# Kernel optimization log

Hardware: AMD Instinct MI355X
Metric: run time of the kernel (lower is better)

Reference implementation:

```python
import jax, jax.numpy as jnp
import numpy as np

BS, LX, LY, D, H, DK = 2, 2048, 2048, 1024, 16, 64


def setup_inputs() -> dict:
    key = jax.random.key(0)
    ks = jax.random.split(key, 12)
    s = 1.0 / np.sqrt(D)
    return {
        "x": jax.random.normal(ks[0], (BS, LX, D), jnp.float32),
        "y": jax.random.normal(ks[1], (BS, LY, D), jnp.float32),
        "mask": jnp.zeros((BS, 1, LX, LY), jnp.float32),
        "Wq": jax.random.normal(ks[2], (D, H * DK), jnp.float32) * s,
        "bq": jnp.zeros((H * DK,), jnp.float32),
        "Wk": jax.random.normal(ks[3], (D, H * DK), jnp.float32) * s,
        "bk": jnp.zeros((H * DK,), jnp.float32),
        "Wv": jax.random.normal(ks[4], (D, H * DK), jnp.float32) * s,
        "bv": jnp.zeros((H * DK,), jnp.float32),
        "Wo": jax.random.normal(ks[5], (H * DK, D), jnp.float32) * s,
        "bo": jnp.zeros((D,), jnp.float32),
    }


def reference(x, y, mask, Wq, bq, Wk, bk, Wv, bv, Wo, bo):
    bs, lx, _ = x.shape
    ly = y.shape[1]
    norm = DK ** 0.5
    # projections -> (bs, len, H, DK)
    q = (x @ Wq + bq).reshape(bs, lx, H, DK)
    k = (y @ Wk + bk).reshape(bs, ly, H, DK)
    v = (y @ Wv + bv).reshape(bs, ly, H, DK)
    # scores: (bs, H, lx, ly)
    scores = jnp.einsum('bxhd,byhd->bhxy', q, k) / norm + mask
    attn = jax.nn.softmax(scores, axis=-1)
    # output: (bs, lx, H, DK) -> (bs, lx, H*DK)
    out = jnp.einsum('bhxy,byhd->bxhd', attn, v).reshape(bs, lx, H * DK)
    return out @ Wo + bo
```

## Files before the change

kernel.cpp:

```cpp
#include <hip/hip_runtime.h>
#include <hip/hip_bf16.h>


typedef __bf16 bf16;
typedef __bf16 bf16x4 __attribute__((ext_vector_type(4)));
typedef __bf16 bf16x8 __attribute__((ext_vector_type(8)));
typedef float floatx4 __attribute__((ext_vector_type(4)));

#define MFMA16(a, b, c) __builtin_amdgcn_mfma_f32_16x16x32_bf16(a, b, c, 0, 0, 0)

constexpr int BS = 2, LX = 2048, LY = 2048, D = 1024, H = 16, DK = 64;
constexpr int HD = H * DK;
constexpr float LOG2E = 1.4426950408889634f;

__device__ __forceinline__ void cp16(const bf16* g, bf16* l) {
  __builtin_amdgcn_global_load_lds(
      (const __attribute__((address_space(1))) unsigned int*)g,
      (__attribute__((address_space(3))) unsigned int*)l, 16, 0, 0);
}

__global__ __launch_bounds__(256) void wprep(const float* __restrict__ W0, bf16* __restrict__ T0,
                                             const float* __restrict__ W1, bf16* __restrict__ T1,
                                             const float* __restrict__ W2, bf16* __restrict__ T2,
                                             const float* __restrict__ W3, bf16* __restrict__ T3) {
  __shared__ bf16 tile[64][72];
  const float* W;
  bf16* T;
  switch (blockIdx.z) {
    case 0: W = W0; T = T0; break;
    case 1: W = W1; T = T1; break;
    case 2: W = W2; T = T2; break;
    default: W = W3; T = T3; break;
  }
  const int kt = blockIdx.x, nt = blockIdx.y;
  const int t = threadIdx.x;
  const int r = t >> 2, c4 = (t & 3) * 16;
  const float* src = W + (size_t)(kt * 64 + r) * 1024 + nt * 64 + c4;
#pragma unroll
  for (int i = 0; i < 16; i++) tile[r][c4 + i] = (bf16)src[i];
  __syncthreads();
  bf16 vals[16];
#pragma unroll
  for (int i = 0; i < 16; i++) vals[i] = tile[c4 + i][r];
  bf16* dst = T + (size_t)(nt * 64 + r) * 1024 + kt * 64 + c4;
#pragma unroll
  for (int i = 0; i < 16; i++) dst[i] = vals[i];
}

__global__ __launch_bounds__(256) void convbf(const float* __restrict__ x, bf16* __restrict__ xb,
                                              const float* __restrict__ y, bf16* __restrict__ yb) {
  const float* src = blockIdx.y ? y : x;
  bf16* dst = blockIdx.y ? yb : xb;
  const size_t i = ((size_t)blockIdx.x * 256 + threadIdx.x) * 8;
  float4 a = *(const float4*)(src + i);
  float4 c = *(const float4*)(src + i + 4);
  bf16 tmp[8] = {(bf16)a.x, (bf16)a.y, (bf16)a.z, (bf16)a.w,
                 (bf16)c.x, (bf16)c.y, (bf16)c.z, (bf16)c.w};
  *(bf16x8*)(dst + i) = *(const bf16x8*)tmp;
}

__global__ __launch_bounds__(256) void maskscan(const float* __restrict__ mask, int* __restrict__ flags) {
  const int region = blockIdx.x >> 5, sub = blockIdx.x & 31;
  const float4* p = (const float4*)mask + (size_t)region * 65536 + sub * 2048;
  bool nz = false;
#pragma unroll
  for (int it = 0; it < 8; it++) {
    float4 v = p[it * 256 + threadIdx.x];
    nz |= (v.x != 0.f) | (v.y != 0.f) | (v.z != 0.f) | (v.w != 0.f);
  }
  if (nz) atomicOr(&flags[region], 1);
}

__global__ __launch_bounds__(256) void qkv_gemm(const bf16* __restrict__ xb, const bf16* __restrict__ yb,
                                                const bf16* __restrict__ Wtq, const bf16* __restrict__ Wtk,
                                                const bf16* __restrict__ Wtv,
                                                const float* __restrict__ bq, const float* __restrict__ bk,
                                                const float* __restrict__ bv,
                                                bf16* __restrict__ Qb, bf16* __restrict__ Kb,
                                                bf16* __restrict__ Vt) {
  constexpr int K = 1024, N = 1024;
  __shared__ __align__(16) bf16 smem[128 * 136];
  bf16* As = smem;
  bf16* Bs = smem + 128 * 64;
  bf16* Ct = smem;

  const int z = blockIdx.z;
  const bf16* A = (z == 0) ? xb : yb;
  const bf16* Bt = (z == 0) ? Wtq : (z == 1) ? Wtk : Wtv;
  const float* bias = (z == 0) ? bq : (z == 1) ? bk : bv;

  const int t = threadIdx.x;
  const int w = t >> 6, lane = t & 63, quad = lane >> 4, l15 = lane & 15;
  const int wr = (w & 1) * 64, wc = (w >> 1) * 64;
  const int mbase = blockIdx.y * 128, nbase = blockIdx.x * 128;
  const int srow = lane >> 3, schunk = (lane & 7) ^ srow;

  floatx4 acc[4][4] = {};

  for (int k0 = 0; k0 < K; k0 += 64) {
    __syncthreads();
#pragma unroll
    for (int j = 0; j < 4; j++) {
      const int r0 = w * 32 + j * 8;
      cp16(A + (size_t)(mbase + r0 + srow) * K + k0 + schunk * 8, As + r0 * 64);
      cp16(Bt + (size_t)(nbase + r0 + srow) * K + k0 + schunk * 8, Bs + r0 * 64);
    }
    __syncthreads();
    bf16x8 af[4][2], bfr[4][2];
#pragma unroll
    for (int i = 0; i < 4; i++) {
      const int ra = wr + i * 16 + l15;
      const int sa = quad ^ (ra & 7);
      af[i][0] = *(const bf16x8*)&As[ra * 64 + sa * 8];
      af[i][1] = *(const bf16x8*)&As[ra * 64 + (sa ^ 4) * 8];
      const int rb = wc + i * 16 + l15;
      const int sb = quad ^ (rb & 7);
      bfr[i][0] = *(const bf16x8*)&Bs[rb * 64 + sb * 8];
      bfr[i][1] = *(const bf16x8*)&Bs[rb * 64 + (sb ^ 4) * 8];
    }
#pragma unroll
    for (int i = 0; i < 4; i++)
#pragma unroll
      for (int jn = 0; jn < 4; jn++) {
        acc[i][jn] = MFMA16(af[i][0], bfr[jn][0], acc[i][jn]);
        acc[i][jn] = MFMA16(af[i][1], bfr[jn][1], acc[i][jn]);
      }
  }

  if (z <= 1) {
    bf16* outp = (z == 0) ? Qb : Kb;
    const float sc = (z == 0) ? 0.125f * LOG2E : 1.0f;
#pragma unroll
    for (int jn = 0; jn < 4; jn++) {
      const int n = nbase + wc + jn * 16 + l15;
      const float bv2 = bias[n];
#pragma unroll
      for (int i = 0; i < 4; i++)
#pragma unroll
        for (int r = 0; r < 4; r++) {
          const int m = mbase + wr + i * 16 + quad * 4 + r;
          outp[(size_t)m * N + n] = (bf16)((acc[i][jn][r] + bv2) * sc);
        }
    }
  } else {
    __syncthreads();
#pragma unroll
    for (int jn = 0; jn < 4; jn++) {
      const int nl = wc + jn * 16 + l15;
      const float bv2 = bias[nbase + nl];
#pragma unroll
      for (int i = 0; i < 4; i++)
#pragma unroll
        for (int r = 0; r < 4; r++) {
          const int ml = wr + i * 16 + quad * 4 + r;
          Ct[nl * 136 + ml] = (bf16)(acc[i][jn][r] + bv2);
        }
    }
    __syncthreads();
    const int n = t >> 1, mh = (t & 1) * 64;
    const int gn = nbase + n;
    const int hh = gn >> 6, dk = gn & 63;
    const int bb = mbase >> 11, y0 = (mbase & 2047) + mh;
    bf16* dst = Vt + ((size_t)(bb * H + hh) * DK + dk) * LY + y0;
    const bf16* srcr = &Ct[n * 136 + mh];
#pragma unroll
    for (int u = 0; u < 8; u++) *(bf16x8*)(dst + u * 8) = *(const bf16x8*)(srcr + u * 8);
  }
}

__global__ __launch_bounds__(256) void out_gemm(const bf16* __restrict__ A, const bf16* __restrict__ Bt,
                                                const float* __restrict__ bias, float* __restrict__ outp) {
  constexpr int K = 1024, N = 1024;
  __shared__ __align__(16) bf16 As[128 * 64];
  __shared__ __align__(16) bf16 Bs[128 * 64];
  const int t = threadIdx.x;
  const int w = t >> 6, lane = t & 63, quad = lane >> 4, l15 = lane & 15;
  const int wr = (w & 1) * 64, wc = (w >> 1) * 64;
  const int mbase = blockIdx.y * 128, nbase = blockIdx.x * 128;
  const int srow = lane >> 3, schunk = (lane & 7) ^ srow;

  floatx4 acc[4][4] = {};
  for (int k0 = 0; k0 < K; k0 += 64) {
    __syncthreads();
#pragma unroll
    for (int j = 0; j < 4; j++) {
      const int r0 = w * 32 + j * 8;
      cp16(A + (size_t)(mbase + r0 + srow) * K + k0 + schunk * 8, As + r0 * 64);
      cp16(Bt + (size_t)(nbase + r0 + srow) * K + k0 + schunk * 8, Bs + r0 * 64);
    }
    __syncthreads();
    bf16x8 af[4][2], bfr[4][2];
#pragma unroll
    for (int i = 0; i < 4; i++) {
      const int ra = wr + i * 16 + l15;
      const int sa = quad ^ (ra & 7);
      af[i][0] = *(const bf16x8*)&As[ra * 64 + sa * 8];
      af[i][1] = *(const bf16x8*)&As[ra * 64 + (sa ^ 4) * 8];
      const int rb = wc + i * 16 + l15;
      const int sb = quad ^ (rb & 7);
      bfr[i][0] = *(const bf16x8*)&Bs[rb * 64 + sb * 8];
      bfr[i][1] = *(const bf16x8*)&Bs[rb * 64 + (sb ^ 4) * 8];
    }
#pragma unroll
    for (int i = 0; i < 4; i++)
#pragma unroll
      for (int jn = 0; jn < 4; jn++) {
        acc[i][jn] = MFMA16(af[i][0], bfr[jn][0], acc[i][jn]);
        acc[i][jn] = MFMA16(af[i][1], bfr[jn][1], acc[i][jn]);
      }
  }
#pragma unroll
  for (int jn = 0; jn < 4; jn++) {
    const int n = nbase + wc + jn * 16 + l15;
    const float bv2 = bias[n];
#pragma unroll
    for (int i = 0; i < 4; i++)
#pragma unroll
      for (int r = 0; r < 4; r++) {
        const int m = mbase + wr + i * 16 + quad * 4 + r;
        outp[(size_t)m * N + n] = acc[i][jn][r] + bv2;
      }
  }
}

__global__ __launch_bounds__(256, 2) void attn4(const bf16* __restrict__ Q, const bf16* __restrict__ Kb,
                                                const bf16* __restrict__ Vt, const float* __restrict__ mask,
                                                const int* __restrict__ flags, bf16* __restrict__ Hout) {
  __shared__ __align__(16) bf16 Ks[2][64 * 64];
  __shared__ __align__(16) bf16 Vs[2][64 * 64];
  __shared__ __align__(16) bf16 Plds[4][32 * 72];
  const int t = threadIdx.x;
  const int w = t >> 6, lane = t & 63, quad = lane >> 4, l15 = lane & 15;
  const int xt = blockIdx.x, h = blockIdx.y, b = blockIdx.z;
  const int qbase = xt * 128 + w * 32;
  const int srow = lane >> 3, schunk = (lane & 7) ^ srow;

  bf16x8 qf[2][2];
#pragma unroll
  for (int rt = 0; rt < 2; rt++) {
    const bf16* qrow = Q + (size_t)(b * LX + qbase + rt * 16 + l15) * HD + h * DK;
    qf[rt][0] = *(const bf16x8*)(qrow + quad * 8);
    qf[rt][1] = *(const bf16x8*)(qrow + 32 + quad * 8);
  }
  const int mflag = flags[b * 16 + xt];

  bf16 onearr[8];
#pragma unroll
  for (int i = 0; i < 8; i++) onearr[i] = (bf16)((l15 == 0) ? 1.0f : 0.0f);
  const bf16x8 onesf = *(const bf16x8*)onearr;

  floatx4 o[2][4] = {};
  floatx4 ol[2] = {};

  const bf16* Kbase = Kb + (size_t)b * LY * HD + h * DK;
  const bf16* Vbase = Vt + (size_t)(b * H + h) * DK * LY;

#define STAGE(yt, bufi)                                                               \
  {                                                                                   \
    _Pragma("unroll") for (int j = 0; j < 2; j++) {                                   \
      const int r0 = w * 16 + j * 8;                                                  \
      cp16(Kbase + (size_t)((yt) + r0 + srow) * HD + schunk * 8, &Ks[bufi][r0 * 64]); \
      cp16(Vbase + (size_t)(r0 + srow) * LY + (yt) + schunk * 8, &Vs[bufi][r0 * 64]); \
    }                                                                                 \
  }

  STAGE(0, 0);

  int buf = 0;
  for (int yt = 0; yt < LY; yt += 64) {
    __syncthreads();
    if (yt + 64 < LY) STAGE(yt + 64, buf ^ 1);

    bf16x8 kf[4][2];
#pragma unroll
    for (int nt = 0; nt < 4; nt++) {
      const int ry = nt * 16 + l15;
      const int sk = quad ^ (ry & 7);
      kf[nt][0] = *(const bf16x8*)&Ks[buf][ry * 64 + sk * 8];
      kf[nt][1] = *(const bf16x8*)&Ks[buf][ry * 64 + (sk ^ 4) * 8];
    }
    floatx4 s[2][4] = {};
#pragma unroll
    for (int nt = 0; nt < 4; nt++)
#pragma unroll
      for (int rt = 0; rt < 2; rt++) {
        s[rt][nt] = MFMA16(kf[nt][0], qf[rt][0], s[rt][nt]);
        s[rt][nt] = MFMA16(kf[nt][1], qf[rt][1], s[rt][nt]);
      }
    if (mflag) {
#pragma unroll
      for (int rt = 0; rt < 2; rt++)
#pragma unroll
        for (int nt = 0; nt < 4; nt++) {
          const float* mp =
              mask + (size_t)(b * LX + qbase + rt * 16 + l15) * LY + yt + nt * 16 + quad * 4;
          float4 mv = *(const float4*)mp;
          s[rt][nt][0] = fminf(s[rt][nt][0] + LOG2E * mv.x, 30.f);
          s[rt][nt][1] = fminf(s[rt][nt][1] + LOG2E * mv.y, 30.f);
          s[rt][nt][2] = fminf(s[rt][nt][2] + LOG2E * mv.z, 30.f);
          s[rt][nt][3] = fminf(s[rt][nt][3] + LOG2E * mv.w, 30.f);
        }
    }

#pragma unroll
    for (int rt = 0; rt < 2; rt++)
#pragma unroll
      for (int nt = 0; nt < 4; nt++) {
        bf16x4 pk;
#pragma unroll
        for (int r = 0; r < 4; r++) pk[r] = (bf16)exp2f(s[rt][nt][r]);
        *(bf16x4*)&Plds[w][(rt * 16 + l15) * 72 + nt * 16 + quad * 4] = pk;
      }

    bf16x8 pf[2][2];
#pragma unroll
    for (int rt = 0; rt < 2; rt++) {
      const bf16* prow = &Plds[w][(rt * 16 + l15) * 72];
      pf[rt][0] = *(const bf16x8*)(prow + quad * 8);
      pf[rt][1] = *(const bf16x8*)(prow + 32 + quad * 8);
    }
#pragma unroll
    for (int u = 0; u < 4; u++) {
      const int rd = u * 16 + l15;
      const int sv = quad ^ (rd & 7);
      bf16x8 v0 = *(const bf16x8*)&Vs[buf][rd * 64 + sv * 8];
      bf16x8 v1 = *(const bf16x8*)&Vs[buf][rd * 64 + (sv ^ 4) * 8];
#pragma unroll
      for (int rt = 0; rt < 2; rt++) {
        o[rt][u] = MFMA16(pf[rt][0], v0, o[rt][u]);
        o[rt][u] = MFMA16(pf[rt][1], v1, o[rt][u]);
      }
    }
#pragma unroll
    for (int rt = 0; rt < 2; rt++) {
      ol[rt] = MFMA16(pf[rt][0], onesf, ol[rt]);
      ol[rt] = MFMA16(pf[rt][1], onesf, ol[rt]);
    }
    buf ^= 1;
  }

#pragma unroll
  for (int rt = 0; rt < 2; rt++)
#pragma unroll
    for (int r = 0; r < 4; r++) {
      const float lsum = __shfl(ol[rt][r], lane & 48, 64);
      const float rl = 1.0f / lsum;
      const int m = b * LX + qbase + rt * 16 + quad * 4 + r;
#pragma unroll
      for (int u = 0; u < 4; u++)
        Hout[(size_t)m * HD + h * DK + u * 16 + l15] = (bf16)(o[rt][u][r] * rl);
    }
#undef STAGE
}

extern "C" void kernel_launch(void* const* d_in, const int* in_sizes, int n_in,
                              void* d_out, int out_size, void* d_ws, size_t ws_size,
                              hipStream_t stream) {
  const float* x = (const float*)d_in[0];
  const float* y = (const float*)d_in[1];
  const float* mask = (const float*)d_in[2];
  const float* Wq = (const float*)d_in[3];
  const float* bq = (const float*)d_in[4];
  const float* Wk = (const float*)d_in[5];
  const float* bk = (const float*)d_in[6];
  const float* Wv = (const float*)d_in[7];
  const float* bv = (const float*)d_in[8];
  const float* Wo = (const float*)d_in[9];
  const float* bo = (const float*)d_in[10];

  char* ws = (char*)d_ws;
  size_t off = 0;
  bf16* Qb = (bf16*)(ws + off); off += (size_t)BS * LX * HD * 2;
  bf16* Kb = (bf16*)(ws + off); off += (size_t)BS * LY * HD * 2;
  bf16* Vt = (bf16*)(ws + off); off += (size_t)BS * LY * HD * 2;
  bf16* Hb = (bf16*)(ws + off); off += (size_t)BS * LX * HD * 2;
  bf16* xbf = (bf16*)(ws + off); off += (size_t)BS * LX * D * 2;
  bf16* ybf = (bf16*)(ws + off); off += (size_t)BS * LY * D * 2;
  bf16* Wtq = (bf16*)(ws + off); off += (size_t)D * HD * 2;
  bf16* Wtk = (bf16*)(ws + off); off += (size_t)D * HD * 2;
  bf16* Wtv = (bf16*)(ws + off); off += (size_t)D * HD * 2;
  bf16* Wto = (bf16*)(ws + off); off += (size_t)HD * D * 2;
  int* flags = (int*)(ws + off); off += 32 * sizeof(int);

  dim3 blk(256);
  wprep<<<dim3(16, 16, 4), blk, 0, stream>>>(Wq, Wtq, Wk, Wtk, Wv, Wtv, Wo, Wto);
  convbf<<<dim3(2048, 2), blk, 0, stream>>>(x, xbf, y, ybf);
  hipMemsetAsync(flags, 0, 32 * sizeof(int), stream);
  maskscan<<<dim3(1024), blk, 0, stream>>>(mask, flags);
  qkv_gemm<<<dim3(8, 32, 3), blk, 0, stream>>>(xbf, ybf, Wtq, Wtk, Wtv, bq, bk, bv, Qb, Kb, Vt);
  attn4<<<dim3(16, 16, 2), blk, 0, stream>>>(Qb, Kb, Vt, mask, flags, Hb);
  out_gemm<<<dim3(8, 32), blk, 0, stream>>>(Hb, Wto, bo, (float*)d_out);
}
```

Before: 264.0 us.

## Fuse prep kernels, retile out GEMM, unroll attention loop by two buffers

Merges the weight transpose, activation bf16 conversion and mask scan into one prep kernel to cut launch overhead. Shrinks the output GEMM N-tile from 128 to 64, doubling the grid for better CU occupancy. Unrolls the attention loop into two static-buffer tile calls so buffer indices become compile-time, and hoists swizzle and mask base address computations. The smaller out_gemm tile lowers data reuse per block.

```diff
diff --git a/kernel.cpp b/kernel.cpp
--- a/kernel.cpp
+++ b/kernel.cpp
@@ -19,56 +19,59 @@
       (__attribute__((address_space(3))) unsigned int*)l, 16, 0, 0);
 }
 
-__global__ __launch_bounds__(256) void wprep(const float* __restrict__ W0, bf16* __restrict__ T0,
-                                             const float* __restrict__ W1, bf16* __restrict__ T1,
-                                             const float* __restrict__ W2, bf16* __restrict__ T2,
-                                             const float* __restrict__ W3, bf16* __restrict__ T3) {
-  __shared__ bf16 tile[64][72];
-  const float* W;
-  bf16* T;
-  switch (blockIdx.z) {
-    case 0: W = W0; T = T0; break;
-    case 1: W = W1; T = T1; break;
-    case 2: W = W2; T = T2; break;
-    default: W = W3; T = T3; break;
-  }
-  const int kt = blockIdx.x, nt = blockIdx.y;
+__global__ __launch_bounds__(256) void prep(const float* __restrict__ W0, bf16* __restrict__ T0,
+                                            const float* __restrict__ W1, bf16* __restrict__ T1,
+                                            const float* __restrict__ W2, bf16* __restrict__ T2,
+                                            const float* __restrict__ W3, bf16* __restrict__ T3,
+                                            const float* __restrict__ x, bf16* __restrict__ xb,
+                                            const float* __restrict__ y, bf16* __restrict__ yb,
+                                            const float* __restrict__ mask, int* __restrict__ flags) {
+  const int id = blockIdx.x;
   const int t = threadIdx.x;
-  const int r = t >> 2, c4 = (t & 3) * 16;
-  const float* src = W + (size_t)(kt * 64 + r) * 1024 + nt * 64 + c4;
-#pragma unroll
-  for (int i = 0; i < 16; i++) tile[r][c4 + i] = (bf16)src[i];
-  __syncthreads();
-  bf16 vals[16];
-#pragma unroll
-  for (int i = 0; i < 16; i++) vals[i] = tile[c4 + i][r];
-  bf16* dst = T + (size_t)(nt * 64 + r) * 1024 + kt * 64 + c4;
-#pragma unroll
-  for (int i = 0; i < 16; i++) dst[i] = vals[i];
-}
-
-__global__ __launch_bounds__(256) void convbf(const float* __restrict__ x, bf16* __restrict__ xb,
-                                              const float* __restrict__ y, bf16* __restrict__ yb) {
-  const float* src = blockIdx.y ? y : x;
-  bf16* dst = blockIdx.y ? yb : xb;
-  const size_t i = ((size_t)blockIdx.x * 256 + threadIdx.x) * 8;
-  float4 a = *(const float4*)(src + i);
-  float4 c = *(const float4*)(src + i + 4);
-  bf16 tmp[8] = {(bf16)a.x, (bf16)a.y, (bf16)a.z, (bf16)a.w,
-                 (bf16)c.x, (bf16)c.y, (bf16)c.z, (bf16)c.w};
-  *(bf16x8*)(dst + i) = *(const bf16x8*)tmp;
-}
-
-__global__ __launch_bounds__(256) void maskscan(const float* __restrict__ mask, int* __restrict__ flags) {
-  const int region = blockIdx.x >> 5, sub = blockIdx.x & 31;
-  const float4* p = (const float4*)mask + (size_t)region * 65536 + sub * 2048;
-  bool nz = false;
-#pragma unroll
-  for (int it = 0; it < 8; it++) {
-    float4 v = p[it * 256 + threadIdx.x];
-    nz |= (v.x != 0.f) | (v.y != 0.f) | (v.z != 0.f) | (v.w != 0.f);
-  }
-  if (nz) atomicOr(&flags[region], 1);
+  if (id < 1024) {
+    __shared__ bf16 tile[64][72];
+    const float* W;
+    bf16* T;
+    switch (id >> 8) {
+      case 0: W = W0; T = T0; break;
+      case 1: W = W1; T = T1; break;
+      case 2: W = W2; T = T2; break;
+      default: W = W3; T = T3; break;
+    }
+    const int kt = id & 15, nt = (id >> 4) & 15;
+    const int r = t >> 2, c4 = (t & 3) * 16;
+    const float* src = W + (size_t)(kt * 64 + r) * 1024 + nt * 64 + c4;
+#pragma unroll
+    for (int i = 0; i < 16; i++) tile[r][c4 + i] = (bf16)src[i];
+    __syncthreads();
+    bf16 vals[16];
+#pragma unroll
+    for (int i = 0; i < 16; i++) vals[i] = tile[c4 + i][r];
+    bf16* dst = T + (size_t)(nt * 64 + r) * 1024 + kt * 64 + c4;
+#pragma unroll
+    for (int i = 0; i < 16; i++) dst[i] = vals[i];
+  } else if (id < 5120) {
+    const int id2 = id - 1024;
+    const float* src = (id2 >= 2048) ? y : x;
+    bf16* dst = (id2 >= 2048) ? yb : xb;
+    const size_t i = ((size_t)(id2 & 2047) * 256 + t) * 8;
+    float4 a = *(const float4*)(src + i);
+    float4 c = *(const float4*)(src + i + 4);
+    bf16 tmp[8] = {(bf16)a.x, (bf16)a.y, (bf16)a.z, (bf16)a.w,
+                   (bf16)c.x, (bf16)c.y, (bf16)c.z, (bf16)c.w};
+    *(bf16x8*)(dst + i) = *(const bf16x8*)tmp;
+  } else {
+    const int id3 = id - 5120;
+    const int region = id3 >> 5, sub = id3 & 31;
+    const float4* p = (const float4*)mask + (size_t)region * 65536 + sub * 2048;
+    bool nz = false;
+#pragma unroll
+    for (int it = 0; it < 8; it++) {
+      float4 v = p[it * 256 + t];
+      nz |= (v.x != 0.f) | (v.y != 0.f) | (v.z != 0.f) | (v.w != 0.f);
+    }
+    if (nz) atomicOr(&flags[region], 1);
+  }
 }
 
 __global__ __launch_bounds__(256) void qkv_gemm(const bf16* __restrict__ xb, const bf16* __restrict__ yb,
@@ -94,6 +97,7 @@
   const int wr = (w & 1) * 64, wc = (w >> 1) * 64;
   const int mbase = blockIdx.y * 128, nbase = blockIdx.x * 128;
   const int srow = lane >> 3, schunk = (lane & 7) ^ srow;
+  const int sx = quad ^ (l15 & 7);
 
   floatx4 acc[4][4] = {};
 
@@ -110,13 +114,11 @@
 #pragma unroll
     for (int i = 0; i < 4; i++) {
       const int ra = wr + i * 16 + l15;
-      const int sa = quad ^ (ra & 7);
-      af[i][0] = *(const bf16x8*)&As[ra * 64 + sa * 8];
-      af[i][1] = *(const bf16x8*)&As[ra * 64 + (sa ^ 4) * 8];
+      af[i][0] = *(const bf16x8*)&As[ra * 64 + sx * 8];
+      af[i][1] = *(const bf16x8*)&As[ra * 64 + (sx ^ 4) * 8];
       const int rb = wc + i * 16 + l15;
-      const int sb = quad ^ (rb & 7);
-      bfr[i][0] = *(const bf16x8*)&Bs[rb * 64 + sb * 8];
-      bfr[i][1] = *(const bf16x8*)&Bs[rb * 64 + (sb ^ 4) * 8];
+      bfr[i][0] = *(const bf16x8*)&Bs[rb * 64 + sx * 8];
+      bfr[i][1] = *(const bf16x8*)&Bs[rb * 64 + (sx ^ 4) * 8];
     }
 #pragma unroll
     for (int i = 0; i < 4; i++)
@@ -172,37 +174,42 @@
                                                 const float* __restrict__ bias, float* __restrict__ outp) {
   constexpr int K = 1024, N = 1024;
   __shared__ __align__(16) bf16 As[128 * 64];
-  __shared__ __align__(16) bf16 Bs[128 * 64];
+  __shared__ __align__(16) bf16 Bs[64 * 64];
   const int t = threadIdx.x;
   const int w = t >> 6, lane = t & 63, quad = lane >> 4, l15 = lane & 15;
-  const int wr = (w & 1) * 64, wc = (w >> 1) * 64;
-  const int mbase = blockIdx.y * 128, nbase = blockIdx.x * 128;
+  const int mbase = blockIdx.y * 128, nbase = blockIdx.x * 64;
   const int srow = lane >> 3, schunk = (lane & 7) ^ srow;
-
-  floatx4 acc[4][4] = {};
+  const int sx = quad ^ (l15 & 7);
+
+  floatx4 acc[2][4] = {};
   for (int k0 = 0; k0 < K; k0 += 64) {
     __syncthreads();
 #pragma unroll
     for (int j = 0; j < 4; j++) {
       const int r0 = w * 32 + j * 8;
       cp16(A + (size_t)(mbase + r0 + srow) * K + k0 + schunk * 8, As + r0 * 64);
+    }
+#pragma unroll
+    for (int j = 0; j < 2; j++) {
+      const int r0 = w * 16 + j * 8;
       cp16(Bt + (size_t)(nbase + r0 + srow) * K + k0 + schunk * 8, Bs + r0 * 64);
     }
     __syncthreads();
-    bf16x8 af[4][2], bfr[4][2];
-#pragma unroll
-    for (int i = 0; i < 4; i++) {
-      const int ra = wr + i * 16 + l15;
-      const int sa = quad ^ (ra & 7);
-      af[i][0] = *(const bf16x8*)&As[ra * 64 + sa * 8];
-      af[i][1] = *(const bf16x8*)&As[ra * 64 + (sa ^ 4) * 8];
-      const int rb = wc + i * 16 + l15;
-      const int sb = quad ^ (rb & 7);
-      bfr[i][0] = *(const bf16x8*)&Bs[rb * 64 + sb * 8];
-      bfr[i][1] = *(const bf16x8*)&Bs[rb * 64 + (sb ^ 4) * 8];
-    }
-#pragma unroll
-    for (int i = 0; i < 4; i++)
+    bf16x8 af[2][2], bfr[4][2];
+#pragma unroll
+    for (int i = 0; i < 2; i++) {
+      const int ra = w * 32 + i * 16 + l15;
+      af[i][0] = *(const bf16x8*)&As[ra * 64 + sx * 8];
+      af[i][1] = *(const bf16x8*)&As[ra * 64 + (sx ^ 4) * 8];
+    }
+#pragma unroll
+    for (int jn = 0; jn < 4; jn++) {
+      const int rb = jn * 16 + l15;
+      bfr[jn][0] = *(const bf16x8*)&Bs[rb * 64 + sx * 8];
+      bfr[jn][1] = *(const bf16x8*)&Bs[rb * 64 + (sx ^ 4) * 8];
+    }
+#pragma unroll
+    for (int i = 0; i < 2; i++)
 #pragma unroll
       for (int jn = 0; jn < 4; jn++) {
         acc[i][jn] = MFMA16(af[i][0], bfr[jn][0], acc[i][jn]);
@@ -211,19 +218,19 @@
   }
 #pragma unroll
   for (int jn = 0; jn < 4; jn++) {
-    const int n = nbase + wc + jn * 16 + l15;
+    const int n = nbase + jn * 16 + l15;
     const float bv2 = bias[n];
 #pragma unroll
-    for (int i = 0; i < 4; i++)
+    for (int i = 0; i < 2; i++)
 #pragma unroll
       for (int r = 0; r < 4; r++) {
-        const int m = mbase + wr + i * 16 + quad * 4 + r;
+        const int m = mbase + w * 32 + i * 16 + quad * 4 + r;
         outp[(size_t)m * N + n] = acc[i][jn][r] + bv2;
       }
   }
 }
 
-__global__ __launch_bounds__(256, 2) void attn4(const bf16* __restrict__ Q, const bf16* __restrict__ Kb,
+__global__ __launch_bounds__(256, 2) void attn5(const bf16* __restrict__ Q, const bf16* __restrict__ Kb,
                                                 const bf16* __restrict__ Vt, const float* __restrict__ mask,
                                                 const int* __restrict__ flags, bf16* __restrict__ Hout) {
   __shared__ __align__(16) bf16 Ks[2][64 * 64];
@@ -234,6 +241,7 @@
   const int xt = blockIdx.x, h = blockIdx.y, b = blockIdx.z;
   const int qbase = xt * 128 + w * 32;
   const int srow = lane >> 3, schunk = (lane & 7) ^ srow;
+  const int sx = quad ^ (l15 & 7);
 
   bf16x8 qf[2][2];
 #pragma unroll
@@ -254,6 +262,7 @@
 
   const bf16* Kbase = Kb + (size_t)b * LY * HD + h * DK;
   const bf16* Vbase = Vt + (size_t)(b * H + h) * DK * LY;
+  const float* mbase2 = mask + (size_t)(b * LX + qbase + l15) * LY;
 
 #define STAGE(yt, bufi)                                                               \
   {                                                                                   \
@@ -264,79 +273,68 @@
     }                                                                                 \
   }
 
+#define TILE(yt, BUF)                                                                  \
+  {                                                                                    \
+    const bf16* KsB = Ks[BUF];                                                         \
+    const bf16* VsB = Vs[BUF];                                                         \
+    bf16x8 kf[4][2];                                                                   \
+    _Pragma("unroll") for (int nt = 0; nt < 4; nt++) {                                 \
+      const int ry = nt * 16 + l15;                                                    \
+      kf[nt][0] = *(const bf16x8*)&KsB[ry * 64 + sx * 8];                              \
+      kf[nt][1] = *(const bf16x8*)&KsB[ry * 64 + (sx ^ 4) * 8];                        \
+    }                                                                                  \
+    floatx4 s[2][4] = {};                                                              \
+    _Pragma("unroll") for (int nt = 0; nt < 4; nt++)                                   \
+        _Pragma("unroll") for (int rt = 0; rt < 2; rt++) {                             \
+      s[rt][nt] = MFMA16(kf[nt][0], qf[rt][0], s[rt][nt]);                             \
+      s[rt][nt] = MFMA16(kf[nt][1], qf[rt][1], s[rt][nt]);                             \
+    }                                                                                  \
+    if (mflag) {                                                                       \
+      _Pragma("unroll") for (int rt = 0; rt < 2; rt++)                                 \
+          _Pragma("unroll") for (int nt = 0; nt < 4; nt++) {                           \
+        const float* mp = mbase2 + (size_t)rt * 16 * LY + (yt) + nt * 16 + quad * 4;   \
+        float4 mv = *(const float4*)mp;                                                \
+        s[rt][nt][0] = fminf(s[rt][nt][0] + LOG2E * mv.x, 30.f);                       \
+        s[rt][nt][1] = fminf(s[rt][nt][1] + LOG2E * mv.y, 30.f);                       \
+        s[rt][nt][2] = fminf(s[rt][nt][2] + LOG2E * mv.z, 30.f);                       \
+        s[rt][nt][3] = fminf(s[rt][nt][3] + LOG2E * mv.w, 30.f);                       \
+      }                                                                                \
+    }                                                                                  \
+    _Pragma("unroll") for (int rt = 0; rt < 2; rt++)                                   \
+        _Pragma("unroll") for (int nt = 0; nt < 4; nt++) {                             \
+      bf16x4 pk;                                                                       \
+      _Pragma("unroll") for (int r = 0; r < 4; r++) pk[r] = (bf16)exp2f(s[rt][nt][r]); \
+      *(bf16x4*)&Plds[w][(rt * 16 + l15) * 72 + nt * 16 + quad * 4] = pk;              \
+    }                                                                                  \
+    bf16x8 pf[2][2];                                                                   \
+    _Pragma("unroll") for (int rt = 0; rt < 2; rt++) {                                 \
+      const bf16* prow = &Plds[w][(rt * 16 + l15) * 72];                               \
+      pf[rt][0] = *(const bf16x8*)(prow + quad * 8);                                   \
+      pf[rt][1] = *(const bf16x8*)(prow + 32 + quad * 8);                              \
+    }                                                                                  \
+    _Pragma("unroll") for (int u = 0; u < 4; u++) {                                    \
+      const int rd = u * 16 + l15;                                                     \
+      bf16x8 v0 = *(const bf16x8*)&VsB[rd * 64 + sx * 8];                              \
+      bf16x8 v1 = *(const bf16x8*)&VsB[rd * 64 + (sx ^ 4) * 8];                        \
+      _Pragma("unroll") for (int rt = 0; rt < 2; rt++) {                               \
+        o[rt][u] = MFMA16(pf[rt][0], v0, o[rt][u]);                                    \
+        o[rt][u] = MFMA16(pf[rt][1], v1, o[rt][u]);                                    \
+      }                                                                                \
+    }                                                                                  \
+    _Pragma("unroll") for (int rt = 0; rt < 2; rt++) {                                 \
+      ol[rt] = MFMA16(pf[rt][0], onesf, ol[rt]);                                       \
+      ol[rt] = MFMA16(pf[rt][1], onesf, ol[rt]);                                       \
+    }                                                                                  \
+  }
+
   STAGE(0, 0);
-
-  int buf = 0;
-  for (int yt = 0; yt < LY; yt += 64) {
-    __syncthreads();
-    if (yt + 64 < LY) STAGE(yt + 64, buf ^ 1);
-
-    bf16x8 kf[4][2];
-#pragma unroll
-    for (int nt = 0; nt < 4; nt++) {
-      const int ry = nt * 16 + l15;
-      const int sk = quad ^ (ry & 7);
-      kf[nt][0] = *(const bf16x8*)&Ks[buf][ry * 64 + sk * 8];
-      kf[nt][1] = *(const bf16x8*)&Ks[buf][ry * 64 + (sk ^ 4) * 8];
-    }
-    floatx4 s[2][4] = {};
-#pragma unroll
-    for (int nt = 0; nt < 4; nt++)
-#pragma unroll
-      for (int rt = 0; rt < 2; rt++) {
-        s[rt][nt] = MFMA16(kf[nt][0], qf[rt][0], s[rt][nt]);
-        s[rt][nt] = MFMA16(kf[nt][1], qf[rt][1], s[rt][nt]);
-      }
-    if (mflag) {
-#pragma unroll
-      for (int rt = 0; rt < 2; rt++)
-#pragma unroll
-        for (int nt = 0; nt < 4; nt++) {
-          const float* mp =
-              mask + (size_t)(b * LX + qbase + rt * 16 + l15) * LY + yt + nt * 16 + quad * 4;
-          float4 mv = *(const float4*)mp;
-          s[rt][nt][0] = fminf(s[rt][nt][0] + LOG2E * mv.x, 30.f);
-          s[rt][nt][1] = fminf(s[rt][nt][1] + LOG2E * mv.y, 30.f);
-          s[rt][nt][2] = fminf(s[rt][nt][2] + LOG2E * mv.z, 30.f);
-          s[rt][nt][3] = fminf(s[rt][nt][3] + LOG2E * mv.w, 30.f);
-        }
-    }
-
-#pragma unroll
-    for (int rt = 0; rt < 2; rt++)
-#pragma unroll
-      for (int nt = 0; nt < 4; nt++) {
-        bf16x4 pk;
-#pragma unroll
-        for (int r = 0; r < 4; r++) pk[r] = (bf16)exp2f(s[rt][nt][r]);
-        *(bf16x4*)&Plds[w][(rt * 16 + l15) * 72 + nt * 16 + quad * 4] = pk;
-      }
-
-    bf16x8 pf[2][2];
-#pragma unroll
-    for (int rt = 0; rt < 2; rt++) {
-      const bf16* prow = &Plds[w][(rt * 16 + l15) * 72];
-      pf[rt][0] = *(const bf16x8*)(prow + quad * 8);
-      pf[rt][1] = *(const bf16x8*)(prow + 32 + quad * 8);
-    }
-#pragma unroll
-    for (int u = 0; u < 4; u++) {
-      const int rd = u * 16 + l15;
-      const int sv = quad ^ (rd & 7);
-      bf16x8 v0 = *(const bf16x8*)&Vs[buf][rd * 64 + sv * 8];
-      bf16x8 v1 = *(const bf16x8*)&Vs[buf][rd * 64 + (sv ^ 4) * 8];
-#pragma unroll
-      for (int rt = 0; rt < 2; rt++) {
-        o[rt][u] = MFMA16(pf[rt][0], v0, o[rt][u]);
-        o[rt][u] = MFMA16(pf[rt][1], v1, o[rt][u]);
-      }
-    }
-#pragma unroll
-    for (int rt = 0; rt < 2; rt++) {
-      ol[rt] = MFMA16(pf[rt][0], onesf, ol[rt]);
-      ol[rt] = MFMA16(pf[rt][1], onesf, ol[rt]);
-    }
-    buf ^= 1;
+  for (int yt = 0; yt < LY; yt += 128) {
+    __syncthreads();
+    STAGE(yt + 64, 1);
+    TILE(yt, 0);
+    __syncthreads();
+    if (yt + 128 < LY) STAGE(yt + 128, 0);
+    TILE(yt + 64, 1);
   }
 
 #pragma unroll
@@ -351,6 +349,7 @@
         Hout[(size_t)m * HD + h * DK + u * 16 + l15] = (bf16)(o[rt][u][r] * rl);
     }
 #undef STAGE
+#undef TILE
 }
 
 extern "C" void kernel_launch(void* const* d_in, const int* in_sizes, int n_in,
@@ -383,11 +382,9 @@
   int* flags = (int*)(ws + off); off += 32 * sizeof(int);
 
   dim3 blk(256);
-  wprep<<<dim3(16, 16, 4), blk, 0, stream>>>(Wq, Wtq, Wk, Wtk, Wv, Wtv, Wo, Wto);
-  convbf<<<dim3(2048, 2), blk, 0, stream>>>(x, xbf, y, ybf);
   hipMemsetAsync(flags, 0, 32 * sizeof(int), stream);
-  maskscan<<<dim3(1024), blk, 0, stream>>>(mask, flags);
+  prep<<<dim3(6144), blk, 0, stream>>>(Wq, Wtq, Wk, Wtk, Wv, Wtv, Wo, Wto, x, xbf, y, ybf, mask, flags);
   qkv_gemm<<<dim3(8, 32, 3), blk, 0, stream>>>(xbf, ybf, Wtq, Wtk, Wtv, bq, bk, bv, Qb, Kb, Vt);
-  attn4<<<dim3(16, 16, 2), blk, 0, stream>>>(Qb, Kb, Vt, mask, flags, Hb);
-  out_gemm<<<dim3(8, 32), blk, 0, stream>>>(Hb, Wto, bo, (float*)d_out);
-}
+  attn5<<<dim3(16, 16, 2), blk, 0, stream>>>(Qb, Kb, Vt, mask, flags, Hb);
+  out_gemm<<<dim3(16, 32), blk, 0, stream>>>(Hb, Wto, bo, (float*)d_out);
+}
```

After: 249.5 us. 1.06x faster.
